# Performance work log

Hardware: AMD Instinct MI355X
Metric: run time of the kernel (lower is better)

Reference implementation:

```python
import jax, jax.numpy as jnp
import numpy as np

HIDDEN = 256   # opt.hidden_dim
NHEADS = 8     # forced by .view(bs, nq, -1, 8)
LVLS = 4       # opt.num_feature_levels
NQ = 300       # opt.real_num_queries
BS = 2
LVL_HWS = [(128, 128), (64, 64), (32, 32), (16, 16)]  # ceil((1024/8)/2**l)
OUT = 7        # roi_align output_size
SR = 2         # fixed sampling_ratio (torchvision default -1 is adaptive/data-dependent)
_STARTS = np.cumsum([0] + [h * w for h, w in LVL_HWS]).tolist()


def setup_inputs():
    key = jax.random.key(0)
    ks = jax.random.split(key, 20)
    def rn(i, shape, s=1.0):
        return jax.random.normal(ks[i], shape, jnp.float32) * s
    total = _STARTS[-1]
    memory = rn(0, (BS, total, HIDDEN))
    tgt = rn(1, (BS, NQ, HIDDEN))
    cxcy = jax.random.uniform(ks[2], (BS, NQ, LVLS, 2), jnp.float32)
    ltrb = jax.random.uniform(ks[3], (BS, NQ, LVLS, 4), jnp.float32) * 0.2 + 0.02
    reference = jnp.concatenate([cxcy, ltrb], axis=-1)  # (bs, nq, lvls, 6)
    level_start_index = jnp.array(_STARTS[:LVLS], jnp.int32)
    C4 = HIDDEN // 4
    params = dict(
        p1_w=rn(4, (HIDDEN, C4), 0.05), p1_b=rn(5, (C4,), 0.05),
        p2_w1=rn(6, (C4 * OUT * OUT, 256), 0.02), p2_b1=rn(7, (256,), 0.02),
        p2_w2=rn(8, (256, 512), 0.02), p2_b2=rn(9, (512,), 0.02),
        p2_w3=rn(10, (512, 512), 0.02), p2_b3=rn(11, (512,), 0.02),
        p2_w4=rn(12, (512, NHEADS * 2), 0.02), p2_b4=rn(13, (NHEADS * 2,), 0.02),
        attn1_w=rn(14, (HIDDEN, HIDDEN * NHEADS), 0.02), attn1_b=rn(15, (HIDDEN * NHEADS,), 0.02),
        attn2_w=rn(16, (HIDDEN, 1), 0.05), attn2_b=rn(17, (1,), 0.05))
    return dict(tgt=tgt, memory=memory, reference=reference,
                level_start_index=level_start_index, **params)


def _roi_align(mem2d, boxes):
    """torchvision roi_align, aligned=True, output 7x7, sampling_ratio=SR.
    mem2d: (B,C,H,W); boxes: (B,nq,4) xyxy in feature coords -> (B,nq,C,7,7)."""
    B, C, H, W = mem2d.shape
    nq = boxes.shape[1]
    fl = mem2d.reshape(B, C, H * W)
    x1, y1, x2, y2 = boxes[..., 0], boxes[..., 1], boxes[..., 2], boxes[..., 3]
    sx, sy = x1 - 0.5, y1 - 0.5                      # aligned=True half-pixel offset
    bw, bh = (x2 - x1) / OUT, (y2 - y1) / OUT
    # sample positions: bin pw, subsample ix -> pw + (ix+0.5)/SR  (pw-major order)
    t = (jnp.arange(OUT, dtype=jnp.float32)[:, None]
         + (jnp.arange(SR, dtype=jnp.float32)[None, :] + 0.5) / SR).reshape(-1)  # (S,)
    S = OUT * SR
    xs = sx[..., None] + bw[..., None] * t           # (B,nq,S)
    ys = sy[..., None] + bh[..., None] * t
    yy = jnp.broadcast_to(ys[:, :, :, None], (B, nq, S, S)).reshape(B, -1)
    xx = jnp.broadcast_to(xs[:, :, None, :], (B, nq, S, S)).reshape(B, -1)
    valid = (yy >= -1.0) & (yy <= H) & (xx >= -1.0) & (xx <= W)
    yc = jnp.clip(yy, 0.0, H - 1.0)
    xc = jnp.clip(xx, 0.0, W - 1.0)
    y0 = jnp.clip(jnp.floor(yc), 0.0, H - 2.0)
    x0 = jnp.clip(jnp.floor(xc), 0.0, W - 2.0)
    ly, lx = yc - y0, xc - x0
    y0i, x0i = y0.astype(jnp.int32), x0.astype(jnp.int32)

    def g(yi, xi):
        return jnp.take_along_axis(fl, (yi * W + xi)[:, None, :], axis=2)  # (B,C,P)

    v = (((1 - ly) * (1 - lx))[:, None] * g(y0i, x0i)
         + ((1 - ly) * lx)[:, None] * g(y0i, x0i + 1)
         + (ly * (1 - lx))[:, None] * g(y0i + 1, x0i)
         + (ly * lx)[:, None] * g(y0i + 1, x0i + 1))
    v = v * valid[:, None, :].astype(v.dtype)
    v = v.reshape(B, C, nq, OUT, SR, OUT, SR).mean(axis=(4, 6))  # bin average
    return v.transpose(0, 2, 1, 3, 4)  # (B,nq,C,7,7)


def _grid_sample(feat, gx, gy):
    """F.grid_sample bilinear, padding_mode='zeros', align_corners=False.
    feat: (N,C,H,W); gx,gy: (N,P) in [-1,1] -> (N,C,P)."""
    N, C, H, W = feat.shape
    fl = feat.reshape(N, C, H * W)
    ix = ((gx + 1.0) * W - 1.0) * 0.5
    iy = ((gy + 1.0) * H - 1.0) * 0.5
    x0, y0 = jnp.floor(ix), jnp.floor(iy)
    lx, ly = ix - x0, iy - y0
    out = jnp.zeros((N, C, gx.shape[1]), feat.dtype)
    for dy, dx, w in ((0, 0, (1 - ly) * (1 - lx)), (0, 1, (1 - ly) * lx),
                      (1, 0, ly * (1 - lx)), (1, 1, ly * lx)):
        xi, yi = x0 + dx, y0 + dy
        m = (xi >= 0) & (xi < W) & (yi >= 0) & (yi < H)
        idx = (jnp.clip(yi, 0, H - 1) * W + jnp.clip(xi, 0, W - 1)).astype(jnp.int32)
        out = out + (w * m)[:, None, :] * jnp.take_along_axis(fl, idx[:, None, :], axis=2)
    return out


def _forward(tgt, memory, ref, p1_w, p1_b, p2_w1, p2_b1, p2_w2, p2_b2,
             p2_w3, p2_b3, p2_w4, p2_b4, attn1_w, attn1_b, attn2_w, attn2_b):
    B, nq = tgt.shape[0], tgt.shape[1]
    gate = jax.nn.sigmoid((tgt @ attn1_w + attn1_b).reshape(B, nq, NHEADS, HIDDEN))
    levels = []
    for lvi in range(LVLS):
        h, w = LVL_HWS[lvi]
        s = _STARTS[lvi]
        mem2d = memory[:, s:s + h * w, :].transpose(0, 2, 1).reshape(B, HIDDEN, h, w)
        r = ref[:, :, lvi]                            # (B,nq,6): cx,cy,l,t,r,b
        cx, cy = r[..., 0], r[..., 1]
        x1 = jnp.clip(cx - r[..., 2], 0.0, 1.0) * w
        y1 = jnp.clip(cy - r[..., 3], 0.0, 1.0) * h
        x2 = jnp.clip(cx + r[..., 4], 0.0, 1.0) * w
        y2 = jnp.clip(cy + r[..., 5], 0.0, 1.0) * h
        boxes = jnp.stack([x1, y1, x2, y2], axis=-1)
        roi = _roi_align(mem2d, boxes)                # (B,nq,C,7,7)
        # point1: 1x1 conv + ReLU, then point2 MLP -> per-head sample offsets
        p = jax.nn.relu(jnp.einsum('bqchw,cd->bqdhw', roi, p1_w) + p1_b[:, None, None])
        p = p.reshape(B, nq, -1)
        p = jax.nn.relu(p @ p2_w1 + p2_b1)
        p = jax.nn.relu(p @ p2_w2 + p2_b2)
        p = jax.nn.relu(p @ p2_w3 + p2_b3)
        pts = jnp.tanh(p @ p2_w4 + p2_b4).reshape(B * nq, NHEADS, 2)
        samp = _grid_sample(roi.reshape(B * nq, HIDDEN, OUT, OUT),
                            pts[..., 0], pts[..., 1])           # (B*nq,C,8)
        samp = samp.reshape(B, nq, HIDDEN, NHEADS).transpose(0, 1, 3, 2)  # (B,nq,8,C)
        levels.append(samp * gate)
    qe = jnp.stack(levels, axis=2).reshape(B, nq, LVLS * NHEADS, HIDDEN)
    wgt = jax.nn.softmax((qe @ attn2_w + attn2_b)[..., 0], axis=-1)  # (B,nq,lvls*heads)
    return (qe * wgt[..., None]).sum(axis=-2)  # (B,nq,C)


def reference(tgt, memory, reference, level_start_index, p1_w, p1_b,
              p2_w1, p2_b1, p2_w2, p2_b2, p2_w3, p2_b3, p2_w4, p2_b4,
              attn1_w, attn1_b, attn2_w, attn2_b):
    # level_start_index is consistent with the static LVL_HWS pyramid
    return _forward(tgt, memory, reference, p1_w, p1_b, p2_w1, p2_b1,
                    p2_w2, p2_b2, p2_w3, p2_b3, p2_w4, p2_b4,
                    attn1_w, attn1_b, attn2_w, attn2_b)
```

## Files before the change

kernel.cpp:

```cpp
#include <hip/hip_runtime.h>
#include <hip/hip_bf16.h>

#define NQ     300
#define NH     8
#define HID    256
#define NLVL   4
#define NCELL  49
#define TOTAL  21760

typedef unsigned short ushort_t;
typedef __attribute__((ext_vector_type(8))) short short8;
typedef __attribute__((ext_vector_type(4))) float floatx4;
typedef __attribute__((ext_vector_type(2))) float floatx2;
typedef __attribute__((ext_vector_type(4))) unsigned int uintx4;

__device__ __forceinline__ float bfbits2f(ushort_t u) {
    union { unsigned int i; float f; } x;
    x.i = ((unsigned int)u) << 16;
    return x.f;
}
__device__ __forceinline__ ushort_t f2bfbits(float v) {
    __hip_bfloat16 h = __float2bfloat16(v);
    return *(ushort_t*)&h;
}
__device__ __forceinline__ unsigned int pack2bf(float a, float b) {
    return (unsigned int)f2bfbits(a) | ((unsigned int)f2bfbits(b) << 16);
}
__device__ __forceinline__ void split_bf(float v, ushort_t& hi, ushort_t& lo) {
    __hip_bfloat16 h = __float2bfloat16(v);
    hi = *(ushort_t*)&h;
    float hv = __bfloat162float(h);
    __hip_bfloat16 l = __float2bfloat16(v - hv);
    lo = *(ushort_t*)&l;
}

__device__ __forceinline__ floatx2 pk_fma(floatx2 a, floatx2 b, floatx2 c) {
    floatx2 d;
    asm("v_pk_fma_f32 %0, %1, %2, %3" : "=v"(d) : "v"(a), "v"(b), "v"(c));
    return d;
}
__device__ __forceinline__ floatx2 unpack2(unsigned int u) {
    union { unsigned int i; float f; } lo, hi;
    lo.i = u << 16;
    hi.i = u & 0xffff0000u;
    return (floatx2){lo.f, hi.f};
}
__device__ __forceinline__ uintx4 ld_async_b128(const ushort_t* p) {
    uintx4 d;
    asm volatile("global_load_dwordx4 %0, %1, off" : "=v"(d) : "v"(p));
    return d;
}

struct Box {
    float sx, sy, bw, bh, Wf;
    int W;
    const ushort_t* memb;
};

__device__ __forceinline__ void load_box(const float* __restrict__ refr,
                                         const ushort_t* __restrict__ mem16,
                                         int r, int lvl, int ch, Box& bx) {
    const int lvl_hw[4] = {128, 64, 32, 16};
    const int lvl_s[4]  = {0, 16384, 20480, 21504};
    const int b = r / NQ;
    bx.W  = lvl_hw[lvl];
    bx.Wf = (float)bx.W;
    const float* rp = refr + ((size_t)r * NLVL + lvl) * 6;
    float cx = rp[0], cy = rp[1];
    float dl = rp[2], dt = rp[3], dr = rp[4], db = rp[5];
    float x1 = fminf(fmaxf(cx - dl, 0.f), 1.f) * bx.Wf;
    float y1 = fminf(fmaxf(cy - dt, 0.f), 1.f) * bx.Wf;
    float x2 = fminf(fmaxf(cx + dr, 0.f), 1.f) * bx.Wf;
    float y2 = fminf(fmaxf(cy + db, 0.f), 1.f) * bx.Wf;
    bx.sx = x1 - 0.5f;
    bx.sy = y1 - 0.5f;
    bx.bw = (x2 - x1) * (1.f / 7.f);
    bx.bh = (y2 - y1) * (1.f / 7.f);
    bx.memb = mem16 + ((size_t)b * TOTAL + lvl_s[lvl]) * HID + ch;
}

__device__ __forceinline__ void tsplit_body(const float* __restrict__ W,
                                            ushort_t* __restrict__ TH,
                                            ushort_t* __restrict__ TL,
                                            int K, int N, int kb, int nb,
                                            int perm, int tid, float (*sm)[65]) {
    for (int e = tid; e < 64 * 64; e += 256) {
        int kk = e >> 6, nn = e & 63;
        int kp = kb + kk;
        int ks = perm ? ((kp & 63) * 49 + (kp >> 6)) : kp;
        sm[kk][nn] = W[(size_t)ks * N + nb + nn];
    }
    __syncthreads();
    for (int e = tid; e < 64 * 64; e += 256) {
        int nn = e >> 6, kk = e & 63;
        ushort_t h, l;
        split_bf(sm[kk][nn], h, l);
        size_t o = (size_t)(nb + nn) * K + kb + kk;
        TH[o] = h; TL[o] = l;
    }
}

__global__ __launch_bounds__(256) void k_prep(
    const float* __restrict__ tgt, ushort_t* __restrict__ tgtH, ushort_t* __restrict__ tgtL,
    const float* __restrict__ a1w, ushort_t* __restrict__ a1wTH, ushort_t* __restrict__ a1wTL,
    const float* __restrict__ w1, ushort_t* __restrict__ w1TH, ushort_t* __restrict__ w1TL,
    const float* __restrict__ w2, ushort_t* __restrict__ w2TH, ushort_t* __restrict__ w2TL,
    const float* __restrict__ w3, ushort_t* __restrict__ w3TH, ushort_t* __restrict__ w3TL,
    const float* __restrict__ p1w, ushort_t* __restrict__ p1wTH, ushort_t* __restrict__ p1wTL,
    const float* __restrict__ memory, ushort_t* __restrict__ mem16) {
    __shared__ float sm[64][65];
    const int tid = threadIdx.x;
    int b = blockIdx.x;
    if (b < 600) {
        int i = b * 256 + tid;
        ushort_t h, l;
        split_bf(tgt[i], h, l);
        tgtH[i] = h; tgtL[i] = l;
    } else if (b < 728) {
        b -= 600;
        tsplit_body(a1w, a1wTH, a1wTL, 256, 2048, (b % 4) * 64, (b / 4) * 64, 0, tid, sm);
    } else if (b < 924) {
        b -= 728;
        tsplit_body(w1, w1TH, w1TL, 3136, 256, (b % 49) * 64, (b / 49) * 64, 1, tid, sm);
    } else if (b < 956) {
        b -= 924;
        tsplit_body(w2, w2TH, w2TL, 256, 512, (b % 4) * 64, (b / 4) * 64, 0, tid, sm);
    } else if (b < 1020) {
        b -= 956;
        tsplit_body(w3, w3TH, w3TL, 512, 512, (b % 8) * 64, (b / 8) * 64, 0, tid, sm);
    } else if (b < 1024) {
        b -= 1020;
        tsplit_body(p1w, p1wTH, p1wTL, 256, 64, b * 64, 0, 0, tid, sm);
    } else {
        b -= 1024;
        size_t i = (size_t)b * 256 + tid;
        float4 v = ((const float4*)memory)[i];
        ushort4 o;
        o.x = f2bfbits(v.x); o.y = f2bfbits(v.y);
        o.z = f2bfbits(v.z); o.w = f2bfbits(v.w);
        ((ushort4*)mem16)[i] = o;
    }
}

template <int EPI, int AX>
__global__ __launch_bounds__(256) void k_gmfma(
    const ushort_t* __restrict__ AH, const ushort_t* __restrict__ AL,
    const ushort_t* __restrict__ WH, const ushort_t* __restrict__ WL,
    const float* __restrict__ bias, float* __restrict__ Cf,
    ushort_t* __restrict__ CH, ushort_t* __restrict__ CL,
    int M, int N, int K, int kchunk) {
    __shared__ ushort_t As[AX ? 1 : 2][64][40];
    __shared__ ushort_t Ws[2][64][40];

    const int tid = threadIdx.x;
    const int m0 = blockIdx.x * 64, n0 = blockIdx.y * 64;
    const int wv = tid >> 6, ln = tid & 63;
    const int row = tid >> 2, kc = tid & 3;
    const int gm = min(m0 + row, M - 1);
    const int gn = n0 + row;
    const int arow = wv * 16 + (ln & 15);
    const int koff = (ln >> 4) * 8;

    int kb = 0, ke = K;
    if (EPI == 3) {
        kb = blockIdx.z * kchunk;
        ke = min(K, kb + kchunk);
    }

    floatx4 acc[4];
#pragma unroll
    for (int t = 0; t < 4; ++t) acc[t] = (floatx4){0.f, 0.f, 0.f, 0.f};

    for (int k0 = kb; k0 < ke; k0 += 32) {
        *(uint4*)&As[0][row][kc * 8] = *(const uint4*)(AH + (size_t)gm * K + k0 + kc * 8);
        if constexpr (!AX)
            *(uint4*)&As[AX ? 0 : 1][row][kc * 8] = *(const uint4*)(AL + (size_t)gm * K + k0 + kc * 8);
        *(uint4*)&Ws[0][row][kc * 8] = *(const uint4*)(WH + (size_t)gn * K + k0 + kc * 8);
        *(uint4*)&Ws[1][row][kc * 8] = *(const uint4*)(WL + (size_t)gn * K + k0 + kc * 8);
        __syncthreads();

        short8 aH = *(short8*)&As[0][arow][koff];
        short8 aL = aH;
        if constexpr (!AX) aL = *(short8*)&As[AX ? 0 : 1][arow][koff];
#pragma unroll
        for (int t = 0; t < 4; ++t) {
            short8 wH = *(short8*)&Ws[0][t * 16 + (ln & 15)][koff];
            short8 wL = *(short8*)&Ws[1][t * 16 + (ln & 15)][koff];
            acc[t] = __builtin_amdgcn_mfma_f32_16x16x32_bf16(aH, wH, acc[t], 0, 0, 0);
            acc[t] = __builtin_amdgcn_mfma_f32_16x16x32_bf16(aH, wL, acc[t], 0, 0, 0);
            if constexpr (!AX)
                acc[t] = __builtin_amdgcn_mfma_f32_16x16x32_bf16(aL, wH, acc[t], 0, 0, 0);
        }
        __syncthreads();
    }

    float* Cpart = (EPI == 3) ? Cf + (size_t)blockIdx.z * M * N : Cf;
#pragma unroll
    for (int t = 0; t < 4; ++t) {
        int n = n0 + t * 16 + (ln & 15);
        float bv = (EPI == 3) ? 0.f : bias[n];
#pragma unroll
        for (int reg = 0; reg < 4; ++reg) {
            int m = m0 + wv * 16 + (ln >> 4) * 4 + reg;
            if (m < M) {
                float v = acc[t][reg] + bv;
                if (EPI == 0) {
                    v = fmaxf(v, 0.f);
                    ushort_t h, l;
                    split_bf(v, h, l);
                    CH[(size_t)m * N + n] = h;
                    CL[(size_t)m * N + n] = l;
                } else if (EPI == 1) {
                    Cf[(size_t)m * N + n] = fmaxf(v, 0.f);
                } else if (EPI == 2) {
                    Cf[(size_t)m * N + n] = 1.f / (1.f + expf(-v));
                } else {
                    Cpart[(size_t)m * N + n] = v;
                }
            }
        }
    }
}

__global__ __launch_bounds__(256) void k_h1red(
    const float* __restrict__ h1p, const float* __restrict__ b1,
    ushort_t* __restrict__ h1H, ushort_t* __restrict__ h1L) {
    const int idx = blockIdx.x * 256 + threadIdx.x;
    const int n = (idx * 4) & 255;
    float4 s = ((const float4*)h1p)[idx];
#pragma unroll
    for (int z = 1; z < 7; ++z) {
        float4 t = ((const float4*)(h1p + (size_t)z * 2400 * 256))[idx];
        s.x += t.x; s.y += t.y; s.z += t.z; s.w += t.w;
    }
    float4 bv = *(const float4*)(b1 + n);
    s.x = fmaxf(s.x + bv.x, 0.f);
    s.y = fmaxf(s.y + bv.y, 0.f);
    s.z = fmaxf(s.z + bv.z, 0.f);
    s.w = fmaxf(s.w + bv.w, 0.f);
    ushort4 H, L;
    split_bf(s.x, H.x, L.x);
    split_bf(s.y, H.y, L.y);
    split_bf(s.z, H.z, L.z);
    split_bf(s.w, H.w, L.w);
    ((ushort4*)h1H)[idx] = H;
    ((ushort4*)h1L)[idx] = L;
}

__global__ __launch_bounds__(256) void k_roi(
    const ushort_t* __restrict__ mem16, const float* __restrict__ refr,
    ushort_t* __restrict__ roi) {
    const int tid  = threadIdx.x;
    const int wave = tid >> 6, lane = tid & 63;
    const int half = lane >> 5;
    const int chv  = (lane & 31) * 8;
    const int bid  = blockIdx.x;

    int lvl, r, klo, khi;
    if (bid < 1200) {
        lvl = 0; r = bid >> 1;
        klo = (bid & 1) ? 13 : 0; khi = (bid & 1) ? 25 : 13;
    } else if (bid < 2400) {
        const int t = bid - 1200;
        lvl = 1; r = t >> 1;
        klo = (t & 1) ? 13 : 0; khi = (t & 1) ? 25 : 13;
    } else if (bid < 3000) {
        lvl = 2; r = bid - 2400; klo = 0; khi = 25;
    } else {
        lvl = 3; r = bid - 3000; klo = 0; khi = 25;
    }
    const int i2 = r * 4 + lvl;

    Box bx;
    load_box(refr, mem16, r, lvl, chv, bx);
    const int rowstride = bx.W * HID;

    ushort_t* rbase = roi + (size_t)i2 * NCELL * HID + chv;

    for (int k = klo + wave; k < khi; k += 4) {
        const int cell = 2 * k + half;
        const int c = (cell < NCELL) ? cell : (NCELL - 1);
        const int ph = c / 7, pw = c % 7;

        uintx4 ld[16];
        float  w[16];
#pragma unroll
        for (int sub = 0; sub < 4; ++sub) {
            const float tys = (float)ph + ((sub >> 1) + 0.5f) * 0.5f;
            const float txs = (float)pw + ((sub & 1) + 0.5f) * 0.5f;
            const float yy = bx.sy + bx.bh * tys;
            const float xx = bx.sx + bx.bw * txs;
            const float vm = (yy >= -1.f && yy <= bx.Wf && xx >= -1.f && xx <= bx.Wf)
                             ? 0.25f : 0.f;
            const float yc  = fminf(fmaxf(yy, 0.f), bx.Wf - 1.f);
            const float xc  = fminf(fmaxf(xx, 0.f), bx.Wf - 1.f);
            const float y0f = fminf(floorf(yc), bx.Wf - 2.f);
            const float x0f = fminf(floorf(xc), bx.Wf - 2.f);
            const float ly = yc - y0f, lx = xc - x0f;
            const int   y0 = (int)y0f, x0 = (int)x0f;
            const ushort_t* p00 = bx.memb + (y0 * bx.W + x0) * HID;
            ld[sub * 4 + 0] = ld_async_b128(p00);
            ld[sub * 4 + 1] = ld_async_b128(p00 + HID);
            ld[sub * 4 + 2] = ld_async_b128(p00 + rowstride);
            ld[sub * 4 + 3] = ld_async_b128(p00 + rowstride + HID);
            const float omy = 1.f - ly, omx = 1.f - lx;
            w[sub * 4 + 0] = vm * omy * omx;
            w[sub * 4 + 1] = vm * omy * lx;
            w[sub * 4 + 2] = vm * ly  * omx;
            w[sub * 4 + 3] = vm * ly  * lx;
        }

        asm volatile("s_waitcnt vmcnt(0)" ::: "memory");
        __builtin_amdgcn_sched_barrier(0);

        floatx2 a01 = (floatx2){0.f, 0.f}, a23 = (floatx2){0.f, 0.f};
        floatx2 a45 = (floatx2){0.f, 0.f}, a67 = (floatx2){0.f, 0.f};
#pragma unroll
        for (int t = 0; t < 16; ++t) {
            const floatx2 wv2 = (floatx2){w[t], w[t]};
            a01 = pk_fma(unpack2(ld[t][0]), wv2, a01);
            a23 = pk_fma(unpack2(ld[t][1]), wv2, a23);
            a45 = pk_fma(unpack2(ld[t][2]), wv2, a45);
            a67 = pk_fma(unpack2(ld[t][3]), wv2, a67);
        }

        if (cell < NCELL) {
            uint4 o;
            o.x = pack2bf(a01.x, a01.y);
            o.y = pack2bf(a23.x, a23.y);
            o.z = pack2bf(a45.x, a45.y);
            o.w = pack2bf(a67.x, a67.y);
            *(uint4*)&rbase[c * HID] = o;
        }
    }
}

__global__ __launch_bounds__(256) void k_fuse(
    const ushort_t* __restrict__ roi, const float* __restrict__ h3,
    const float* __restrict__ w4, const float* __restrict__ b4,
    const float* __restrict__ gate, const float* __restrict__ w,
    const float* __restrict__ bias, float* __restrict__ out) {
    __shared__ float sm_qe[32 * HID];
    __shared__ float sm_pts[64];
    __shared__ float sm_hd[32][4];
    __shared__ float sm_l[32];
    __shared__ float sm_e[32];

    const int tid = threadIdx.x;
    const int r = blockIdx.x;

    float* sm_h3 = sm_qe;
    {
        const float4* src = (const float4*)(h3 + (size_t)r * 4 * 512);
        float4* dst = (float4*)sm_h3;
        for (int i = tid; i < 512; i += 256) dst[i] = src[i];
    }
    __syncthreads();

    {
        const int o = tid >> 2, s = tid & 3;
        const int row = o >> 4, col = o & 15;
        float part = 0.f;
        const int kb = s * 128;
        for (int k = kb; k < kb + 128; ++k)
            part += sm_h3[row * 512 + k] * w4[k * 16 + col];
        part += __shfl_down(part, 2);
        part += __shfl_down(part, 1);
        if (s == 0) sm_pts[row * 16 + col] = tanhf(part + b4[col]);
    }
    __syncthreads();

    if (tid < 32) {
        int lvl = tid >> 3, h = tid & 7;
        float gx = sm_pts[lvl * 16 + h * 2];
        float gy = sm_pts[lvl * 16 + h * 2 + 1];
        float ix = ((gx + 1.f) * 7.f - 1.f) * 0.5f;
        float iy = ((gy + 1.f) * 7.f - 1.f) * 0.5f;
        float x0f = floorf(ix), y0f = floorf(iy);
        sm_hd[tid][0] = x0f;
        sm_hd[tid][1] = y0f;
        sm_hd[tid][2] = ix - x0f;
        sm_hd[tid][3] = iy - y0f;
    }
    __syncthreads();

    const float* grow = gate + (size_t)r * 2048;
#pragma unroll
    for (int j = 0; j < 32; ++j) {
        int lvl = j >> 3, h = j & 7;
        const ushort_t* rbase = roi + ((size_t)r * 4 + lvl) * NCELL * HID;
        float x0f = sm_hd[j][0], y0f = sm_hd[j][1];
        float lx = sm_hd[j][2], ly = sm_hd[j][3];
        int x0 = (int)x0f, y0 = (int)y0f;
        float v = 0.f;
#pragma unroll
        for (int dy = 0; dy < 2; ++dy) {
            int yi = y0 + dy;
            if (yi < 0 || yi >= 7) continue;
            float wy = dy ? ly : 1.f - ly;
#pragma unroll
            for (int dx = 0; dx < 2; ++dx) {
                int xi = x0 + dx;
                if (xi < 0 || xi >= 7) continue;
                float wx = dx ? lx : 1.f - lx;
                v += wy * wx * bfbits2f(rbase[(yi * 7 + xi) * HID + tid]);
            }
        }
        sm_qe[j * HID + tid] = v * grow[h * HID + tid];
    }
    __syncthreads();

    const int j = tid >> 3, sub = tid & 7;
    float part = 0.f;
    const int cbase = sub * 32;
    for (int c = 0; c < 32; ++c) part += sm_qe[j * HID + cbase + c] * w[cbase + c];
    part += __shfl_down(part, 4);
    part += __shfl_down(part, 2);
    part += __shfl_down(part, 1);
    if (sub == 0) sm_l[j] = part + bias[0];
    __syncthreads();
    if (tid < 32) {
        float m = -1e30f;
        for (int i = 0; i < 32; ++i) m = fmaxf(m, sm_l[i]);
        sm_e[tid] = expf(sm_l[tid] - m);
    }
    __syncthreads();
    float denom = 0.f;
    for (int i = 0; i < 32; ++i) denom += sm_e[i];
    float inv = 1.f / denom;
    float acc = 0.f;
    for (int jj = 0; jj < 32; ++jj) acc += sm_qe[jj * HID + tid] * sm_e[jj];
    out[(size_t)r * HID + tid] = acc * inv;
}

extern "C" void kernel_launch(void* const* d_in, const int* in_sizes, int n_in,
                              void* d_out, int out_size, void* d_ws, size_t ws_size,
                              hipStream_t stream) {
    const float* tgt    = (const float*)d_in[0];
    const float* memory = (const float*)d_in[1];
    const float* refr   = (const float*)d_in[2];
    const float* p1w = (const float*)d_in[4];
    const float* p1b = (const float*)d_in[5];
    const float* w1  = (const float*)d_in[6];
    const float* b1  = (const float*)d_in[7];
    const float* w2  = (const float*)d_in[8];
    const float* b2  = (const float*)d_in[9];
    const float* w3  = (const float*)d_in[10];
    const float* b3  = (const float*)d_in[11];
    const float* w4  = (const float*)d_in[12];
    const float* b4  = (const float*)d_in[13];
    const float* a1w = (const float*)d_in[14];
    const float* a1b = (const float*)d_in[15];
    const float* a2w = (const float*)d_in[16];
    const float* a2b = (const float*)d_in[17];
    float* out = (float*)d_out;

    size_t off = 0;
    auto alloc = [&](size_t bytes) {
        void* p = (char*)d_ws + off;
        off += (bytes + 255) & ~(size_t)255;
        return p;
    };
    float*    gate  = (float*)alloc((size_t)600 * 2048 * 4);
    ushort_t* mem16 = (ushort_t*)alloc((size_t)2 * TOTAL * HID * 2);
    ushort_t* roi   = (ushort_t*)alloc((size_t)2400 * NCELL * HID * 2);
    ushort_t* pHb   = (ushort_t*)alloc((size_t)2400 * 3136 * 2);
    ushort_t* pLb   = (ushort_t*)alloc((size_t)2400 * 3136 * 2);
    float*    h1p   = (float*)alloc((size_t)7 * 2400 * 256 * 4);
    ushort_t* h1H   = (ushort_t*)alloc((size_t)2400 * 256 * 2);
    ushort_t* h1L   = (ushort_t*)alloc((size_t)2400 * 256 * 2);
    ushort_t* h2H   = (ushort_t*)alloc((size_t)2400 * 512 * 2);
    ushort_t* h2L   = (ushort_t*)alloc((size_t)2400 * 512 * 2);
    float*    h3    = (float*)alloc((size_t)2400 * 512 * 4);
    ushort_t* tgtH  = (ushort_t*)alloc((size_t)600 * 256 * 2);
    ushort_t* tgtL  = (ushort_t*)alloc((size_t)600 * 256 * 2);
    ushort_t* a1wTH = (ushort_t*)alloc((size_t)2048 * 256 * 2);
    ushort_t* a1wTL = (ushort_t*)alloc((size_t)2048 * 256 * 2);
    ushort_t* w1TH  = (ushort_t*)alloc((size_t)256 * 3136 * 2);
    ushort_t* w1TL  = (ushort_t*)alloc((size_t)256 * 3136 * 2);
    ushort_t* w2TH  = (ushort_t*)alloc((size_t)512 * 256 * 2);
    ushort_t* w2TL  = (ushort_t*)alloc((size_t)512 * 256 * 2);
    ushort_t* w3TH  = (ushort_t*)alloc((size_t)512 * 512 * 2);
    ushort_t* w3TL  = (ushort_t*)alloc((size_t)512 * 512 * 2);
    ushort_t* p1wTH = (ushort_t*)alloc((size_t)64 * 256 * 2);
    ushort_t* p1wTL = (ushort_t*)alloc((size_t)64 * 256 * 2);

    hipLaunchKernelGGL(k_prep, dim3(11904), dim3(256), 0, stream,
                       tgt, tgtH, tgtL, a1w, a1wTH, a1wTL,
                       w1, w1TH, w1TL, w2, w2TH, w2TL, w3, w3TH, w3TL,
                       p1w, p1wTH, p1wTL, memory, mem16);

    hipLaunchKernelGGL((k_gmfma<2, 0>), dim3(10, 32), dim3(256), 0, stream,
                       tgtH, tgtL, a1wTH, a1wTL, a1b, gate, (ushort_t*)0, (ushort_t*)0,
                       600, 2048, 256, 0);
    hipLaunchKernelGGL(k_roi, dim3(3600), dim3(256), 0, stream, mem16, refr, roi);
    hipLaunchKernelGGL((k_gmfma<0, 1>), dim3(1838, 1), dim3(256), 0, stream,
                       roi, (ushort_t*)0, p1wTH, p1wTL, p1b, (float*)0, pHb, pLb,
                       2400 * NCELL, 64, 256, 0);
    hipLaunchKernelGGL((k_gmfma<3, 0>), dim3(38, 4, 7), dim3(256), 0, stream,
                       pHb, pLb, w1TH, w1TL, (float*)0, h1p, (ushort_t*)0, (ushort_t*)0,
                       2400, 256, 3136, 448);
    hipLaunchKernelGGL(k_h1red, dim3(600), dim3(256), 0, stream, h1p, b1, h1H, h1L);
    hipLaunchKernelGGL((k_gmfma<0, 0>), dim3(38, 8), dim3(256), 0, stream,
                       h1H, h1L, w2TH, w2TL, b2, (float*)0, h2H, h2L, 2400, 512, 256, 0);
    hipLaunchKernelGGL((k_gmfma<1, 0>), dim3(38, 8), dim3(256), 0, stream,
                       h2H, h2L, w3TH, w3TL, b3, h3, (ushort_t*)0, (ushort_t*)0,
                       2400, 512, 512, 0);
    hipLaunchKernelGGL(k_fuse, dim3(600), dim3(256), 0, stream,
                       roi, h3, w4, b4, gate, a2w, a2b, out);
}
```

Before: 340.3 us.

## Add weight-resident MFMA GEMM kernel and use it for four GEMMs

Adds a new GEMM kernel that loads the whole K-extent of a weight N-tile (hi/lo bf16 split) into XOR-swizzled shared memory once. Each wave then streams its A rows straight from global memory, with a 128-row M tile per block. Four of the existing k_gmfma launches (attn1 gate, p1 projection, w2, w3) are switched to it, with new grid shapes. The aim is to avoid re-staging weights through LDS in every K loop and to cut synchronisation. In exchange, A operands are read from global without reuse through LDS, and large LDS use may lower occupancy.

```diff
diff --git a/kernel.cpp b/kernel.cpp
--- a/kernel.cpp
+++ b/kernel.cpp
@@ -222,6 +222,97 @@
     }
 }
 
+template <int EPI, int AX, int KK, int NT>
+__global__ __launch_bounds__(256) void k_wres(
+    const ushort_t* __restrict__ AH, const ushort_t* __restrict__ AL,
+    const ushort_t* __restrict__ WH, const ushort_t* __restrict__ WL,
+    const float* __restrict__ bias, float* __restrict__ Cf,
+    ushort_t* __restrict__ CH, ushort_t* __restrict__ CL,
+    int M, int N, int nbm) {
+    constexpr int KC = KK / 8;
+    __shared__ ushort_t Wls[2 * NT * KK];
+
+    const int tid = threadIdx.x;
+    const int m0 = (blockIdx.x % nbm) * 128;
+    const int n0 = (blockIdx.x / nbm) * NT;
+
+    {
+        const uint4* sH = (const uint4*)(WH + (size_t)n0 * KK);
+        const uint4* sL = (const uint4*)(WL + (size_t)n0 * KK);
+        uint4* d = (uint4*)Wls;
+        for (int i = tid; i < NT * KC; i += 256) {
+            const int nn = i / KC, kk = i % KC;
+            const int sw = nn * KC + (kk ^ (nn & 7));
+            d[sw] = sH[i];
+            d[NT * KC + sw] = sL[i];
+        }
+    }
+    __syncthreads();
+
+    const int wv = tid >> 6, ln = tid & 63;
+    const int koff = (ln >> 4) * 8, nidx = ln & 15;
+    const size_t a0 = (size_t)min(m0 + wv * 16 + (ln & 15), M - 1) * KK;
+    const size_t a1 = (size_t)min(m0 + 64 + wv * 16 + (ln & 15), M - 1) * KK;
+
+    floatx4 acc[2][NT / 16];
+#pragma unroll
+    for (int s = 0; s < 2; ++s)
+#pragma unroll
+        for (int t = 0; t < NT / 16; ++t) acc[s][t] = (floatx4){0.f, 0.f, 0.f, 0.f};
+
+    for (int k0 = 0; k0 < KK; k0 += 32) {
+        short8 a0H = *(const short8*)(AH + a0 + k0 + koff);
+        short8 a1H = *(const short8*)(AH + a1 + k0 + koff);
+        short8 a0L = a0H, a1L = a1H;
+        if constexpr (!AX) {
+            a0L = *(const short8*)(AL + a0 + k0 + koff);
+            a1L = *(const short8*)(AL + a1 + k0 + koff);
+        }
+        const int kc = (k0 + koff) >> 3;
+#pragma unroll
+        for (int t = 0; t < NT / 16; ++t) {
+            const int wrow = t * 16 + nidx;
+            const int swr = wrow * KC + (kc ^ (wrow & 7));
+            short8 wHf = *(const short8*)((const uint4*)Wls + swr);
+            short8 wLf = *(const short8*)((const uint4*)Wls + NT * KC + swr);
+            acc[0][t] = __builtin_amdgcn_mfma_f32_16x16x32_bf16(a0H, wHf, acc[0][t], 0, 0, 0);
+            acc[0][t] = __builtin_amdgcn_mfma_f32_16x16x32_bf16(a0H, wLf, acc[0][t], 0, 0, 0);
+            if constexpr (!AX)
+                acc[0][t] = __builtin_amdgcn_mfma_f32_16x16x32_bf16(a0L, wHf, acc[0][t], 0, 0, 0);
+            acc[1][t] = __builtin_amdgcn_mfma_f32_16x16x32_bf16(a1H, wHf, acc[1][t], 0, 0, 0);
+            acc[1][t] = __builtin_amdgcn_mfma_f32_16x16x32_bf16(a1H, wLf, acc[1][t], 0, 0, 0);
+            if constexpr (!AX)
+                acc[1][t] = __builtin_amdgcn_mfma_f32_16x16x32_bf16(a1L, wHf, acc[1][t], 0, 0, 0);
+        }
+    }
+
+#pragma unroll
+    for (int s = 0; s < 2; ++s)
+#pragma unroll
+        for (int t = 0; t < NT / 16; ++t) {
+            const int n = n0 + t * 16 + nidx;
+            const float bv = bias[n];
+#pragma unroll
+            for (int reg = 0; reg < 4; ++reg) {
+                const int m = m0 + s * 64 + wv * 16 + (ln >> 4) * 4 + reg;
+                if (m < M) {
+                    float v = acc[s][t][reg] + bv;
+                    if constexpr (EPI == 0) {
+                        v = fmaxf(v, 0.f);
+                        ushort_t h, l;
+                        split_bf(v, h, l);
+                        CH[(size_t)m * N + n] = h;
+                        CL[(size_t)m * N + n] = l;
+                    } else if constexpr (EPI == 1) {
+                        Cf[(size_t)m * N + n] = fmaxf(v, 0.f);
+                    } else {
+                        Cf[(size_t)m * N + n] = 1.f / (1.f + expf(-v));
+                    }
+                }
+            }
+        }
+}
+
 __global__ __launch_bounds__(256) void k_h1red(
     const float* __restrict__ h1p, const float* __restrict__ b1,
     ushort_t* __restrict__ h1H, ushort_t* __restrict__ h1L) {
@@ -490,22 +581,22 @@
                        w1, w1TH, w1TL, w2, w2TH, w2TL, w3, w3TH, w3TL,
                        p1w, p1wTH, p1wTL, memory, mem16);
 
-    hipLaunchKernelGGL((k_gmfma<2, 0>), dim3(10, 32), dim3(256), 0, stream,
+    hipLaunchKernelGGL((k_wres<2, 0, 256, 64>), dim3(5 * 32), dim3(256), 0, stream,
                        tgtH, tgtL, a1wTH, a1wTL, a1b, gate, (ushort_t*)0, (ushort_t*)0,
-                       600, 2048, 256, 0);
+                       600, 2048, 5);
     hipLaunchKernelGGL(k_roi, dim3(3600), dim3(256), 0, stream, mem16, refr, roi);
-    hipLaunchKernelGGL((k_gmfma<0, 1>), dim3(1838, 1), dim3(256), 0, stream,
+    hipLaunchKernelGGL((k_wres<0, 1, 256, 64>), dim3(919), dim3(256), 0, stream,
                        roi, (ushort_t*)0, p1wTH, p1wTL, p1b, (float*)0, pHb, pLb,
-                       2400 * NCELL, 64, 256, 0);
+                       2400 * NCELL, 64, 919);
     hipLaunchKernelGGL((k_gmfma<3, 0>), dim3(38, 4, 7), dim3(256), 0, stream,
                        pHb, pLb, w1TH, w1TL, (float*)0, h1p, (ushort_t*)0, (ushort_t*)0,
                        2400, 256, 3136, 448);
     hipLaunchKernelGGL(k_h1red, dim3(600), dim3(256), 0, stream, h1p, b1, h1H, h1L);
-    hipLaunchKernelGGL((k_gmfma<0, 0>), dim3(38, 8), dim3(256), 0, stream,
-                       h1H, h1L, w2TH, w2TL, b2, (float*)0, h2H, h2L, 2400, 512, 256, 0);
-    hipLaunchKernelGGL((k_gmfma<1, 0>), dim3(38, 8), dim3(256), 0, stream,
+    hipLaunchKernelGGL((k_wres<0, 0, 256, 64>), dim3(19 * 8), dim3(256), 0, stream,
+                       h1H, h1L, w2TH, w2TL, b2, (float*)0, h2H, h2L, 2400, 512, 19);
+    hipLaunchKernelGGL((k_wres<1, 0, 512, 32>), dim3(19 * 16), dim3(256), 0, stream,
                        h2H, h2L, w3TH, w3TL, b3, h3, (ushort_t*)0, (ushort_t*)0,
-                       2400, 512, 512, 0);
+                       2400, 512, 19);
     hipLaunchKernelGGL(k_fuse, dim3(600), dim3(256), 0, stream,
                        roi, h3, w4, b4, gate, a2w, a2b, out);
 }
```

New measurement: 337.4 us. About the same (-0.9%).
